# Performance work log

Measured on AMD Instinct MI355X. Metric: run time of the kernel, lower is better.

The kernel has to match this reference:

```python
import jax, jax.numpy as jnp
import numpy as np

TEMPORAL_LAMBDA = 0.1


def setup_inputs() -> dict:
    key = jax.random.key(0)
    k1, k2 = jax.random.split(key)
    preds = jax.random.normal(k1, (2, 8, 16, 128, 256), dtype=jnp.float32)   # (B,T,M,H,W)
    target = jax.random.normal(k2, (2, 8, 1, 128, 256), dtype=jnp.float32)   # (B,T,1,H,W)
    return {"preds": preds, "target": target}


def reference(preds, target):
    # CRPS = E[|X - y|] - 0.5 * E[|X - X'|]
    term1 = jnp.abs(preds - target).mean(axis=2)                 # (B,T,H,W)
    # pairwise |x_i - x_j| over ensemble dim (M x M broadcast, as in original)
    pairwise = jnp.abs(preds[:, :, :, None] - preds[:, :, None, :])  # (B,T,M,M,H,W)
    term2 = 0.5 * pairwise.mean(axis=(2, 3))                     # (B,T,H,W)
    crps = term1 - term2
    # temporal consistency penalty (temporal_lambda > 0 branch)
    crps = crps.mean(axis=1)                                     # (B,H,W)
    temporal_diff = preds[:, 1:] - preds[:, :-1]                 # (B,T-1,M,H,W)
    temporal_penalty = jnp.abs(temporal_diff).mean(axis=(1, 2))  # (B,H,W)
    crps = crps + TEMPORAL_LAMBDA * temporal_penalty
    crps = crps[:, None, None]                                   # (B,1,1,H,W)
    return crps.mean()                                           # reduction='mean'
```

## Files before the change

### kernel.cpp

```cpp
#include <hip/hip_runtime.h>

#define HW    32768
#define T_DIM 8
#define E_DIM 16
#define NPOS  65536
#define BLK   256
#define KPAIR 4
#define NTHREADS (2 * KPAIR * HW)
#define NBLK  (NTHREADS / BLK)

__device__ __forceinline__ float block_reduce_256(float v, float* lds) {
#pragma unroll
    for (int off = 32; off; off >>= 1)
        v += __shfl_down(v, off, 64);
    int lane = threadIdx.x & 63;
    int wid  = threadIdx.x >> 6;
    if (lane == 0) lds[wid] = v;
    __syncthreads();
    return lds[0] + lds[1] + lds[2] + lds[3];
}

__device__ __forceinline__ float crps_term(const float* p, float tgt) {
    float t1 = 0.f;
#pragma unroll
    for (int e = 0; e < E_DIM; ++e)
        t1 += fabsf(p[e] - tgt);
    float s = 0.f;
#pragma unroll
    for (int i = 0; i < E_DIM; ++i)
#pragma unroll
        for (int j = i + 1; j < E_DIM; ++j)
            s += fabsf(p[i] - p[j]);
    return t1 * (1.f / 16.f) - s * (1.f / 256.f);
}

__global__ __launch_bounds__(BLK) void crps_partial(const float* __restrict__ preds,
                                                    const float* __restrict__ target,
                                                    float* __restrict__ partials) {
    const int n  = blockIdx.x * BLK + threadIdx.x;
    const int hw = n & (HW - 1);
    const int k  = (n >> 15) & (KPAIR - 1);
    const int b  = n >> 17;
    const int t0 = 2 * k;

    const float* pb = preds  + (size_t)b * T_DIM * E_DIM * HW + hw;
    const float* tb = target + (size_t)b * T_DIM * HW + hw;

    float cur0[E_DIM], cur1[E_DIM];
#pragma unroll
    for (int e = 0; e < E_DIM; ++e)
        cur0[e] = pb[((size_t)(t0 * E_DIM) + e) * HW];
#pragma unroll
    for (int e = 0; e < E_DIM; ++e)
        cur1[e] = pb[((size_t)((t0 + 1) * E_DIM) + e) * HW];

    const float tgt0 = tb[(size_t)t0 * HW];
    const float tgt1 = tb[(size_t)(t0 + 1) * HW];

    float tacc = 0.f;
    if (k > 0) {
#pragma unroll
        for (int e = 0; e < E_DIM; ++e) {
            float pv = pb[((size_t)((t0 - 1) * E_DIM) + e) * HW];
            tacc += fabsf(cur0[e] - pv);
        }
    }
#pragma unroll
    for (int e = 0; e < E_DIM; ++e)
        tacc += fabsf(cur1[e] - cur0[e]);

    float acc = crps_term(cur0, tgt0) + crps_term(cur1, tgt1);

    float v = acc * (1.f / 8.f) + tacc * (0.1f / 112.f);

    __shared__ float lds[4];
    float bsum = block_reduce_256(v, lds);
    if (threadIdx.x == 0)
        partials[blockIdx.x] = bsum;
}

__global__ __launch_bounds__(BLK) void crps_final(const float* __restrict__ partials,
                                                  float* __restrict__ out) {
    float v = 0.f;
#pragma unroll
    for (int i = 0; i < NBLK / BLK; ++i)
        v += partials[i * BLK + threadIdx.x];
    __shared__ float lds[4];
    float total = block_reduce_256(v, lds);
    if (threadIdx.x == 0)
        out[0] = total * (1.f / (float)NPOS);
}

extern "C" void kernel_launch(void* const* d_in, const int* in_sizes, int n_in,
                              void* d_out, int out_size, void* d_ws, size_t ws_size,
                              hipStream_t stream) {
    const float* preds  = (const float*)d_in[0];
    const float* target = (const float*)d_in[1];
    float* out      = (float*)d_out;
    float* partials = (float*)d_ws;

    crps_partial<<<NBLK, BLK, 0, stream>>>(preds, target, partials);
    crps_final<<<1, BLK, 0, stream>>>(partials, out);
}
```

Measured before the change: 13.68 us.

## Share adjacent timestep ensemble values via LDS instead of reloading from global

Each block now covers 64 spatial positions across all four time-step pairs, one wave per pair. Waves pass their second-timestep ensemble values through shared memory to the next wave, so the temporal-difference term no longer reloads the previous timestep from global memory. This cuts global traffic by roughly a sixth. In exchange it adds a block-wide barrier and LDS writes and reads, and the wave-per-pair mapping changes the memory access pattern.

```diff
diff --git a/kernel.cpp b/kernel.cpp
--- a/kernel.cpp
+++ b/kernel.cpp
@@ -5,9 +5,7 @@
 #define E_DIM 16
 #define NPOS  65536
 #define BLK   256
-#define KPAIR 4
-#define NTHREADS (2 * KPAIR * HW)
-#define NBLK  (NTHREADS / BLK)
+#define NBLK  1024
 
 __device__ __forceinline__ float block_reduce_256(float v, float* lds) {
 #pragma unroll
@@ -37,44 +35,51 @@
 __global__ __launch_bounds__(BLK) void crps_partial(const float* __restrict__ preds,
                                                     const float* __restrict__ target,
                                                     float* __restrict__ partials) {
-    const int n  = blockIdx.x * BLK + threadIdx.x;
-    const int hw = n & (HW - 1);
-    const int k  = (n >> 15) & (KPAIR - 1);
-    const int b  = n >> 17;
-    const int t0 = 2 * k;
+    const int lane = threadIdx.x & 63;
+    const int w    = threadIdx.x >> 6;
+    const int grp  = blockIdx.x & 511;
+    const int b    = blockIdx.x >> 9;
+    const int hw   = grp * 64 + lane;
+    const int t0   = 2 * w;
 
-    const float* pb = preds  + (size_t)b * T_DIM * E_DIM * HW + hw;
-    const float* tb = target + (size_t)b * T_DIM * HW + hw;
+    const float* pb = preds  + hw;
+    const float* tb = target + hw;
 
     float cur0[E_DIM], cur1[E_DIM];
 #pragma unroll
     for (int e = 0; e < E_DIM; ++e)
-        cur0[e] = pb[((size_t)(t0 * E_DIM) + e) * HW];
+        cur0[e] = pb[((size_t)((b * T_DIM + t0) * E_DIM) + e) * HW];
 #pragma unroll
     for (int e = 0; e < E_DIM; ++e)
-        cur1[e] = pb[((size_t)((t0 + 1) * E_DIM) + e) * HW];
+        cur1[e] = pb[((size_t)((b * T_DIM + t0 + 1) * E_DIM) + e) * HW];
+    const float tgt0 = tb[(size_t)(b * T_DIM + t0) * HW];
+    const float tgt1 = tb[(size_t)(b * T_DIM + t0 + 1) * HW];
 
-    const float tgt0 = tb[(size_t)t0 * HW];
-    const float tgt1 = tb[(size_t)(t0 + 1) * HW];
+    __shared__ float xch[3][E_DIM][64];
+    if (w < 3) {
+#pragma unroll
+        for (int e = 0; e < E_DIM; ++e)
+            xch[w][e][lane] = cur1[e];
+    }
 
+    float acc = crps_term(cur0, tgt0) + crps_term(cur1, tgt1);
     float tacc = 0.f;
-    if (k > 0) {
-#pragma unroll
-        for (int e = 0; e < E_DIM; ++e) {
-            float pv = pb[((size_t)((t0 - 1) * E_DIM) + e) * HW];
-            tacc += fabsf(cur0[e] - pv);
-        }
-    }
 #pragma unroll
     for (int e = 0; e < E_DIM; ++e)
         tacc += fabsf(cur1[e] - cur0[e]);
 
-    float acc = crps_term(cur0, tgt0) + crps_term(cur1, tgt1);
+    __syncthreads();
+
+    if (w > 0) {
+#pragma unroll
+        for (int e = 0; e < E_DIM; ++e)
+            tacc += fabsf(cur0[e] - xch[w - 1][e][lane]);
+    }
 
     float v = acc * (1.f / 8.f) + tacc * (0.1f / 112.f);
 
-    __shared__ float lds[4];
-    float bsum = block_reduce_256(v, lds);
+    __shared__ float rlds[4];
+    float bsum = block_reduce_256(v, rlds);
     if (threadIdx.x == 0)
         partials[blockIdx.x] = bsum;
 }
```

New measurement: 20.81 us. 52.1% more time.
